# Kernel tuning notes

Hardware: AMD Instinct MI355X
Metric: run time of the kernel (lower is better)

## Reference

```python
import jax, jax.numpy as jnp
import numpy as np


def setup_inputs() -> dict:
    key = jax.random.key(0)
    k1, k2 = jax.random.split(key)
    N = 8192
    # Inputs are lower-triangular by contract of the original module.
    A = jnp.tril(jax.random.normal(k1, (N, N), dtype=jnp.float32))
    B = jnp.tril(jax.random.normal(k2, (N, N), dtype=jnp.float32))
    return {"A": A, "B": B}


def reference(A, B):
    # C = tril(A @ B): product of two lower-triangular matrices is lower
    # triangular; the original applies tril to zero numerical garbage in the
    # strictly-upper part (and to enforce it in the fallback path).
    return jnp.tril(jnp.matmul(A, B))
```

## Files before the change

### kernel.cpp

```cpp
#include <hip/hip_runtime.h>
#include <hip/hip_bf16.h>
#include <type_traits>
#include <utility>


static constexpr int MATN = 8192;

typedef __attribute__((ext_vector_type(8))) short  s8v;
typedef __attribute__((ext_vector_type(4))) short  s4h;
typedef __attribute__((ext_vector_type(8))) __bf16 b8v;
typedef __attribute__((ext_vector_type(4))) float  f4v;

template <typename V, typename = void>
struct mfma_ok : std::false_type {};
template <typename V>
struct mfma_ok<V, std::void_t<decltype(__builtin_amdgcn_mfma_f32_16x16x32_bf16(
    std::declval<V>(), std::declval<V>(), std::declval<f4v>(), 0, 0, 0))>>
    : std::true_type {};
using abv = std::conditional_t<mfma_ok<b8v>::value, b8v, s8v>;

__device__ __forceinline__ short f2bf(float f) {
  unsigned u = __builtin_bit_cast(unsigned, f);
  unsigned r = (u + 0x7fffu + ((u >> 16) & 1u)) >> 16;
  return (short)r;
}

__device__ __forceinline__ void async16(void* lds, const void* g) {
  __builtin_amdgcn_global_load_lds(
      (const __attribute__((address_space(1))) unsigned int*)g,
      (__attribute__((address_space(3))) unsigned int*)lds, 16, 0, 0);
}

__device__ __forceinline__ int tri_decode(int id) {
  int k = (int)((sqrtf(8.0f * (float)id + 1.0f) - 1.0f) * 0.5f);
  while ((k + 1) * (k + 2) / 2 <= id) k++;
  while (k * (k + 1) / 2 > id) k--;
  return k;
}

__global__ __launch_bounds__(256) void convert_A_k(const float* __restrict__ A,
                                                   short* __restrict__ Abf) {
  int gid  = blockIdx.x * 256 + threadIdx.x;
  int base = gid * 8;
  int row  = base >> 13;
  int col  = base & 8191;
  s8v o = {};
  if (col <= row) {
    f4v v0 = *(const f4v*)&A[base];
    f4v v1 = *(const f4v*)&A[base + 4];
#pragma unroll
    for (int i = 0; i < 4; i++) { o[i] = f2bf(v0[i]); o[4 + i] = f2bf(v1[i]); }
  }
  *(s8v*)&Abf[base] = o;
}

__global__ __launch_bounds__(256) void transpose_B_k(const float* __restrict__ B,
                                                     short* __restrict__ Bt) {
  __shared__ __align__(16) short T[64 * 68];
  int k0 = blockIdx.x * 64, n0 = blockIdx.y * 64;
  int tid = threadIdx.x;
  if (k0 + 63 < n0) {
    s8v z = {};
#pragma unroll
    for (int t = 0; t < 2; t++) {
      int c = t * 256 + tid;
      int n = c >> 3, kg = c & 7;
      *(s8v*)&Bt[(size_t)(n0 + n) * MATN + k0 + kg * 8] = z;
    }
    return;
  }
#pragma unroll
  for (int t = 0; t < 4; t++) {
    int c = t * 256 + tid;
    int k = c >> 4, cn = c & 15;
    s4h o = {};
    if (n0 + cn * 4 <= k0 + k) {
      f4v v = *(const f4v*)&B[(size_t)(k0 + k) * MATN + n0 + cn * 4];
#pragma unroll
      for (int i = 0; i < 4; i++) o[i] = f2bf(v[i]);
    }
    int cs = cn ^ (2 * (k >> 3));
    *(s4h*)&T[k * 68 + cs * 4] = o;
  }
  __syncthreads();
#pragma unroll
  for (int t = 0; t < 2; t++) {
    int c = t * 256 + tid;
    int n = c >> 3, kg = c & 7;
    int nn = n ^ (kg * 8);
    s8v o;
#pragma unroll
    for (int i = 0; i < 8; i++) o[i] = T[(kg * 8 + i) * 68 + nn];
    *(s8v*)&Bt[(size_t)(n0 + n) * MATN + k0 + kg * 8] = o;
  }
}

__global__ __launch_bounds__(256) void gemm_tril(const short* __restrict__ Abf,
                                                 const short* __restrict__ Btb,
                                                 float* __restrict__ C) {
  int id = blockIdx.x;
  int tid = threadIdx.x;
  int bi, bj;
  if (id < 2304) {
    int s = id >> 6;
    int t = tri_decode(s);
    int J = s - t * (t + 1) / 2;
    int I = J + 7 - t;
    int li = 7 - ((id >> 3) & 7);
    int lj = id & 7;
    bi = I * 8 + li;
    bj = J * 8 + lj;
  } else {
    int q = id - 2304;
    int s = q >> 6;
    int r = tri_decode(s);
    int I = s - r * (r + 1) / 2;
    int J = r + 1;
    bi = I * 8 + ((q >> 3) & 7);
    bj = J * 8 + (q & 7);
  }

  if (bi < bj) {
    f4v z = {};
    size_t base = (size_t)bi * 128 * MATN + (size_t)bj * 128;
#pragma unroll
    for (int t = 0; t < 16; t++) {
      int c = t * 256 + tid;
      int r2 = c >> 5, cc = (c & 31) * 4;
      *(f4v*)&C[base + (size_t)r2 * MATN + cc] = z;
    }
    return;
  }

  __shared__ __align__(16) short As[128 * 32];
  __shared__ __align__(16) short Bs[128 * 32];

  int wave = tid >> 6, lane = tid & 63;
  int quad = lane >> 4, ln = lane & 15;
  int wm = wave >> 1, wn = wave & 1;

  int row0 = bi * 128, col0 = bj * 128;
  f4v acc[4][4] = {};

  int r0 = tid >> 2, c0 = (tid & 3) * 8;
  int r1 = 64 + r0;
  char* lA0 = (char*)As + wave * 1024;
  char* lA1 = (char*)As + 4096 + wave * 1024;
  char* lB0 = (char*)Bs + wave * 1024;
  char* lB1 = (char*)Bs + 4096 + wave * 1024;

  int kend = (bi + 1) * 128;
  for (int kt = col0; kt < kend; kt += 32) {
    __syncthreads();
    async16(lA0, &Abf[(size_t)(row0 + r0) * MATN + kt + c0]);
    async16(lA1, &Abf[(size_t)(row0 + r1) * MATN + kt + c0]);
    async16(lB0, &Btb[(size_t)(col0 + r0) * MATN + kt + c0]);
    async16(lB1, &Btb[(size_t)(col0 + r1) * MATN + kt + c0]);
    __syncthreads();

    abv a[4], b[4];
#pragma unroll
    for (int t = 0; t < 4; t++) {
      a[t] = *(const abv*)&As[(wm * 64 + t * 16 + ln) * 32 + quad * 8];
      b[t] = *(const abv*)&Bs[(wn * 64 + t * 16 + ln) * 32 + quad * 8];
    }
#pragma unroll
    for (int tm = 0; tm < 4; tm++)
#pragma unroll
      for (int tn = 0; tn < 4; tn++)
        acc[tm][tn] = __builtin_amdgcn_mfma_f32_16x16x32_bf16(
            a[tm], b[tn], acc[tm][tn], 0, 0, 0);
  }

  bool diag = (bi == bj);
#pragma unroll
  for (int tm = 0; tm < 4; tm++) {
    int grb = row0 + wm * 64 + tm * 16 + quad * 4;
#pragma unroll
    for (int tn = 0; tn < 4; tn++) {
      int gc = col0 + wn * 64 + tn * 16 + ln;
#pragma unroll
      for (int r = 0; r < 4; r++) {
        int gr = grb + r;
        float v = acc[tm][tn][r];
        if (diag && gr < gc) v = 0.0f;
        C[(size_t)gr * MATN + gc] = v;
      }
    }
  }
}

__global__ __launch_bounds__(256) void gemm_tril_f32(const float* __restrict__ A,
                                                     const float* __restrict__ B,
                                                     float* __restrict__ C) {
  int bj = blockIdx.x, bi = blockIdx.y;
  int tid = threadIdx.x;
  int row0 = bi * 64, col0 = bj * 64;
  if (bi < bj) {
    f4v z = {};
#pragma unroll
    for (int t = 0; t < 4; t++) {
      int c = t * 256 + tid;
      int r = c >> 4, cc = (c & 15) * 4;
      *(f4v*)&C[(size_t)(row0 + r) * MATN + col0 + cc] = z;
    }
    return;
  }
  __shared__ float As[64][17];
  __shared__ float Bs[16][65];
  int tx = tid & 15, ty = tid >> 4;
  float acc[4][4] = {};
  int kendf = (bi + 1) * 64;
  for (int kt = col0; kt < kendf; kt += 16) {
    __syncthreads();
#pragma unroll
    for (int t = 0; t < 4; t++) {
      int c = t * 256 + tid;
      int r = c >> 4, k = c & 15;
      As[r][k] = A[(size_t)(row0 + r) * MATN + kt + k];
    }
#pragma unroll
    for (int t = 0; t < 4; t++) {
      int c = t * 256 + tid;
      int k = c >> 6, n = c & 63;
      Bs[k][n] = B[(size_t)(kt + k) * MATN + col0 + n];
    }
    __syncthreads();
#pragma unroll
    for (int k = 0; k < 16; k++) {
      float av[4], bv[4];
#pragma unroll
      for (int i = 0; i < 4; i++) av[i] = As[ty * 4 + i][k];
#pragma unroll
      for (int j = 0; j < 4; j++) bv[j] = Bs[k][tx * 4 + j];
#pragma unroll
      for (int i = 0; i < 4; i++)
#pragma unroll
        for (int j = 0; j < 4; j++) acc[i][j] += av[i] * bv[j];
    }
  }
#pragma unroll
  for (int i = 0; i < 4; i++)
#pragma unroll
    for (int j = 0; j < 4; j++) {
      int gr = row0 + ty * 4 + i, gc = col0 + tx * 4 + j;
      C[(size_t)gr * MATN + gc] = (gr >= gc) ? acc[i][j] : 0.0f;
    }
}

extern "C" void kernel_launch(void* const* d_in, const int* in_sizes, int n_in,
                              void* d_out, int out_size, void* d_ws, size_t ws_size,
                              hipStream_t stream) {
  const float* A = (const float*)d_in[0];
  const float* B = (const float*)d_in[1];
  float* C = (float*)d_out;

  const size_t need = 2ull * MATN * MATN * sizeof(short);
  if (ws_size >= need) {
    short* Abf = (short*)d_ws;
    short* Btb = Abf + (size_t)MATN * MATN;
    convert_A_k<<<(MATN * (size_t)MATN) / 8 / 256, 256, 0, stream>>>(A, Abf);
    transpose_B_k<<<dim3(MATN / 64, MATN / 64), 256, 0, stream>>>(B, Btb);
    gemm_tril<<<4096, 256, 0, stream>>>(Abf, Btb, C);
  } else {
    gemm_tril_f32<<<dim3(MATN / 64, MATN / 64), 256, 0, stream>>>(A, B, C);
  }
}
```

Before: 898.5 us.

## Rewrite triangular GEMM with 256x256 tiles and a 4-stage software pipeline

After: 765.3 us. -14.8%, faster.

```diff
diff --git a/kernel.cpp b/kernel.cpp
--- a/kernel.cpp
+++ b/kernel.cpp
@@ -44,6 +44,7 @@
   int base = gid * 8;
   int row  = base >> 13;
   int col  = base & 8191;
+  if (col > row && (row >> 8) != (col >> 8)) return;
   s8v o = {};
   if (col <= row) {
     f4v v0 = *(const f4v*)&A[base];
@@ -60,12 +61,14 @@
   int k0 = blockIdx.x * 64, n0 = blockIdx.y * 64;
   int tid = threadIdx.x;
   if (k0 + 63 < n0) {
-    s8v z = {};
-#pragma unroll
-    for (int t = 0; t < 2; t++) {
-      int c = t * 256 + tid;
-      int n = c >> 3, kg = c & 7;
-      *(s8v*)&Bt[(size_t)(n0 + n) * MATN + k0 + kg * 8] = z;
+    if ((k0 >> 8) == (n0 >> 8)) {
+      s8v z = {};
+#pragma unroll
+      for (int t = 0; t < 2; t++) {
+        int c = t * 256 + tid;
+        int n = c >> 3, kg = c & 7;
+        *(s8v*)&Bt[(size_t)(n0 + n) * MATN + k0 + kg * 8] = z;
+      }
     }
     return;
   }
@@ -95,94 +98,166 @@
   }
 }
 
-__global__ __launch_bounds__(256) void gemm_tril(const short* __restrict__ Abf,
-                                                 const short* __restrict__ Btb,
-                                                 float* __restrict__ C) {
-  int id = blockIdx.x;
+template <int SA, int C>
+__device__ __forceinline__ void lda4(const char* L, int aoff, abv (&a)[4]) {
+#pragma unroll
+  for (int m = 0; m < 4; m++)
+    a[m] = *(const abv*)(L + SA * 16384 + (C * 64 + m * 16) * 64 + aoff);
+}
+template <int SB>
+__device__ __forceinline__ void ldb4(const char* L, int boff, abv (&b)[4]) {
+#pragma unroll
+  for (int n = 0; n < 4; n++)
+    b[n] = *(const abv*)(L + 65536 + SB * 16384 + n * 1024 + boff);
+}
+template <int C>
+__device__ __forceinline__ void mfma16(const abv (&a)[4], const abv (&b)[4],
+                                       f4v (&acc)[8][4]) {
+#pragma unroll
+  for (int m = 0; m < 4; m++)
+#pragma unroll
+    for (int n = 0; n < 4; n++)
+      acc[C * 4 + m][n] = __builtin_amdgcn_mfma_f32_16x16x32_bf16(
+          a[m], b[n], acc[C * 4 + m][n], 0, 0, 0);
+}
+__device__ __forceinline__ void phase_mid() {
+  __builtin_amdgcn_sched_barrier(0);
+  __builtin_amdgcn_s_barrier();
+  __builtin_amdgcn_sched_barrier(0);
+  __builtin_amdgcn_s_setprio(1);
+}
+template <bool VM6>
+__device__ __forceinline__ void phase_end() {
+  __builtin_amdgcn_s_setprio(0);
+  __builtin_amdgcn_sched_barrier(0);
+  if constexpr (VM6) asm volatile("s_waitcnt vmcnt(6)" ::: "memory");
+  __builtin_amdgcn_s_barrier();
+  __builtin_amdgcn_sched_barrier(0);
+}
+
+#define STAGE_A(S, KT, KK)                                                   \
+  {                                                                          \
+    int kc_ = kstart + (KT) * 64 + (KK) * 32 + csw;                          \
+    async16(LW + (S) * 16384, Abf + gA + kc_);                               \
+    async16(LW + (S) * 16384 + 8192,                                         \
+            Abf + gA + (size_t)128 * MATN + kc_);                            \
+  }
+#define STAGE_B(S, KT, KK)                                                   \
+  {                                                                          \
+    int kc_ = kstart + (KT) * 64 + (KK) * 32 + csw;                          \
+    async16(LW + 65536 + (S) * 16384, Btb + gB + kc_);                       \
+    async16(LW + 65536 + (S) * 16384 + 8192,                                 \
+            Btb + gB + (size_t)128 * MATN + kc_);                            \
+  }
+
+__global__ __launch_bounds__(512) void gemm_tril256(const short* __restrict__ Abf,
+                                                    const short* __restrict__ Btb,
+                                                    float* __restrict__ C) {
+  int id  = blockIdx.x;
   int tid = threadIdx.x;
   int bi, bj;
-  if (id < 2304) {
-    int s = id >> 6;
-    int t = tri_decode(s);
-    int J = s - t * (t + 1) / 2;
-    int I = J + 7 - t;
-    int li = 7 - ((id >> 3) & 7);
-    int lj = id & 7;
-    bi = I * 8 + li;
-    bj = J * 8 + lj;
+  if (id < 528) {
+    int g = tri_decode(id) + 1;
+    int j = id - (g - 1) * g / 2;
+    bi = j + 32 - g;
+    bj = j;
   } else {
-    int q = id - 2304;
-    int s = q >> 6;
-    int r = tri_decode(s);
-    int I = s - r * (r + 1) / 2;
-    int J = r + 1;
-    bi = I * 8 + ((q >> 3) & 7);
-    bj = J * 8 + (q & 7);
-  }
+    int q = id - 528;
+    int r = tri_decode(q);
+    bi = q - r * (r + 1) / 2;
+    bj = r + 1;
+  }
+
+  int row0 = bi << 8, col0 = bj << 8;
 
   if (bi < bj) {
     f4v z = {};
-    size_t base = (size_t)bi * 128 * MATN + (size_t)bj * 128;
-#pragma unroll
-    for (int t = 0; t < 16; t++) {
-      int c = t * 256 + tid;
-      int r2 = c >> 5, cc = (c & 31) * 4;
+    size_t base = (size_t)row0 * MATN + col0;
+#pragma unroll
+    for (int t = 0; t < 32; t++) {
+      int c = t * 512 + tid;
+      int r2 = c >> 6, cc = (c & 63) * 4;
       *(f4v*)&C[base + (size_t)r2 * MATN + cc] = z;
     }
     return;
   }
 
-  __shared__ __align__(16) short As[128 * 32];
-  __shared__ __align__(16) short Bs[128 * 32];
+  __shared__ __align__(16) short LDS[65536];
 
   int wave = tid >> 6, lane = tid & 63;
   int quad = lane >> 4, ln = lane & 15;
-  int wm = wave >> 1, wn = wave & 1;
-
-  int row0 = bi * 128, col0 = bj * 128;
-  f4v acc[4][4] = {};
-
-  int r0 = tid >> 2, c0 = (tid & 3) * 8;
-  int r1 = 64 + r0;
-  char* lA0 = (char*)As + wave * 1024;
-  char* lA1 = (char*)As + 4096 + wave * 1024;
-  char* lB0 = (char*)Bs + wave * 1024;
-  char* lB1 = (char*)Bs + 4096 + wave * 1024;
-
-  int kend = (bi + 1) * 128;
-  for (int kt = col0; kt < kend; kt += 32) {
-    __syncthreads();
-    async16(lA0, &Abf[(size_t)(row0 + r0) * MATN + kt + c0]);
-    async16(lA1, &Abf[(size_t)(row0 + r1) * MATN + kt + c0]);
-    async16(lB0, &Btb[(size_t)(col0 + r0) * MATN + kt + c0]);
-    async16(lB1, &Btb[(size_t)(col0 + r1) * MATN + kt + c0]);
-    __syncthreads();
-
-    abv a[4], b[4];
-#pragma unroll
-    for (int t = 0; t < 4; t++) {
-      a[t] = *(const abv*)&As[(wm * 64 + t * 16 + ln) * 32 + quad * 8];
-      b[t] = *(const abv*)&Bs[(wn * 64 + t * 16 + ln) * 32 + quad * 8];
-    }
-#pragma unroll
-    for (int tm = 0; tm < 4; tm++)
-#pragma unroll
-      for (int tn = 0; tn < 4; tn++)
-        acc[tm][tn] = __builtin_amdgcn_mfma_f32_16x16x32_bf16(
-            a[tm], b[tn], acc[tm][tn], 0, 0, 0);
-  }
+  int wm = wave >> 2, wn = wave & 3;
+
+  const char* L = (const char*)LDS;
+  char* LW = (char*)LDS + wave * 1024;
+
+  int chunk = (quad ^ ((ln >> 1) & 3)) << 4;
+  int aoff = (wm * 128 + ln) * 64 + chunk;
+  int boff = (wn * 64 + ln) * 64 + chunk;
+
+  int csw = (((lane & 3) ^ ((lane >> 3) & 3)) << 3);
+  size_t gA = (size_t)(row0 + wave * 16 + (lane >> 2)) * MATN;
+  size_t gB = (size_t)(col0 + wave * 16 + (lane >> 2)) * MATN;
+
+  int kstart = col0;
+  int NT = (bi + 1 - bj) << 2;
+
+  f4v acc[8][4] = {};
+
+  STAGE_A(0, 0, 0); STAGE_B(0, 0, 0);
+  STAGE_A(1, 0, 1); STAGE_B(1, 0, 1);
+  STAGE_A(2, 1, 0); STAGE_B(2, 1, 0);
+  STAGE_B(3, 1, 1);
+  asm volatile("s_waitcnt vmcnt(6)" ::: "memory");
+  __builtin_amdgcn_s_barrier();
+  __builtin_amdgcn_sched_barrier(0);
+
+  abv a[4], b[4];
+  for (int kt = 0; kt < NT; kt += 2) {
+    int k2 = (kt + 2 < NT) ? kt + 2 : 0;
+    int k3 = (kt + 3 < NT) ? kt + 3 : 0;
+    ldb4<0>(L, boff, b);
+    lda4<0, 0>(L, aoff, a);
+    STAGE_A(3, kt + 1, 1);
+    phase_mid(); mfma16<0>(a, b, acc); phase_end<false>();
+    lda4<0, 1>(L, aoff, a);
+    STAGE_B(0, k2, 0);
+    phase_mid(); mfma16<1>(a, b, acc); phase_end<false>();
+    ldb4<1>(L, boff, b);
+    lda4<1, 0>(L, aoff, a);
+    STAGE_A(0, k2, 0);
+    phase_mid(); mfma16<0>(a, b, acc); phase_end<false>();
+    lda4<1, 1>(L, aoff, a);
+    STAGE_B(1, k2, 1);
+    phase_mid(); mfma16<1>(a, b, acc); phase_end<true>();
+    ldb4<2>(L, boff, b);
+    lda4<2, 0>(L, aoff, a);
+    STAGE_A(1, k2, 1);
+    phase_mid(); mfma16<0>(a, b, acc); phase_end<false>();
+    lda4<2, 1>(L, aoff, a);
+    STAGE_B(2, k3, 0);
+    phase_mid(); mfma16<1>(a, b, acc); phase_end<false>();
+    ldb4<3>(L, boff, b);
+    lda4<3, 0>(L, aoff, a);
+    STAGE_A(2, k3, 0);
+    phase_mid(); mfma16<0>(a, b, acc); phase_end<false>();
+    lda4<3, 1>(L, aoff, a);
+    STAGE_B(3, k3, 1);
+    phase_mid(); mfma16<1>(a, b, acc); phase_end<true>();
+  }
+  asm volatile("s_waitcnt vmcnt(0)" ::: "memory");
 
   bool diag = (bi == bj);
 #pragma unroll
-  for (int tm = 0; tm < 4; tm++) {
-    int grb = row0 + wm * 64 + tm * 16 + quad * 4;
-#pragma unroll
-    for (int tn = 0; tn < 4; tn++) {
-      int gc = col0 + wn * 64 + tn * 16 + ln;
+  for (int m = 0; m < 8; m++) {
+    int grb = row0 + wm * 128 + m * 16 + quad * 4;
+#pragma unroll
+    for (int n = 0; n < 4; n++) {
+      int gc = col0 + wn * 64 + n * 16 + ln;
 #pragma unroll
       for (int r = 0; r < 4; r++) {
         int gr = grb + r;
-        float v = acc[tm][tn][r];
+        float v = acc[m][n][r];
         if (diag && gr < gc) v = 0.0f;
         C[(size_t)gr * MATN + gc] = v;
       }
@@ -261,7 +336,7 @@
     short* Btb = Abf + (size_t)MATN * MATN;
     convert_A_k<<<(MATN * (size_t)MATN) / 8 / 256, 256, 0, stream>>>(A, Abf);
     transpose_B_k<<<dim3(MATN / 64, MATN / 64), 256, 0, stream>>>(B, Btb);
-    gemm_tril<<<4096, 256, 0, stream>>>(Abf, Btb, C);
+    gemm_tril256<<<1024, 512, 0, stream>>>(Abf, Btb, C);
   } else {
     gemm_tril_f32<<<dim3(MATN / 64, MATN / 64), 256, 0, stream>>>(A, B, C);
   }
```
